# Kernel tuning notes

Hardware: AMD Instinct MI355X
Metric: run time of the kernel (lower is better)

Reference implementation:

```python
import jax, jax.numpy as jnp
import numpy as np

B, N, D_IN, D_OUT, H = 2, 2048, 1024, 1024, 16
HD = D_OUT // H


def setup_inputs() -> dict:
    key = jax.random.key(0)
    ks = jax.random.split(key, 6)
    s_in = 1.0 / np.sqrt(D_IN)
    s_out = 1.0 / np.sqrt(D_OUT)
    return {
        "x": jax.random.normal(ks[0], (B, N, D_IN), dtype=jnp.float32),
        "Wq": jax.random.uniform(ks[1], (D_IN, D_OUT), jnp.float32, -s_in, s_in),
        "Wk": jax.random.uniform(ks[2], (D_IN, D_OUT), jnp.float32, -s_in, s_in),
        "Wv": jax.random.uniform(ks[3], (D_IN, D_OUT), jnp.float32, -s_in, s_in),
        "Wo": jax.random.uniform(ks[4], (D_OUT, D_OUT), jnp.float32, -s_out, s_out),
        "bo": jax.random.uniform(ks[5], (D_OUT,), jnp.float32, -s_out, s_out),
    }


def reference(x, Wq, Wk, Wv, Wo, bo):
    b, n, _ = x.shape
    # project and split heads: [b, n, d_out] -> [b, h, n, hd]
    def heads(w):
        return w.reshape(b, n, H, HD).transpose(0, 2, 1, 3)
    q = heads(x @ Wq)
    k = heads(x @ Wk)
    v = heads(x @ Wv)
    # materialized causal attention (dropout rate 0.0 -> identity)
    scores = jnp.einsum("bhqd,bhkd->bhqk", q, k)
    causal = jnp.tril(jnp.ones((n, n), dtype=bool))  # keep lower triangle
    scores = jnp.where(causal, scores, -jnp.inf)
    attn = jax.nn.softmax(scores / np.sqrt(HD), axis=-1)
    ctx = jnp.einsum("bhqk,bhkd->bhqd", attn, v)
    ctx = ctx.transpose(0, 2, 1, 3).reshape(b, n, D_OUT)
    return ctx @ Wo + bo
```

## Files before the change

kernel.cpp:

```cpp
#include <hip/hip_runtime.h>
#include <math.h>
#include <stdint.h>

#define B_ 2
#define N_ 2048
#define D_ 1024
#define H_ 16
#define HD_ 64
#define M_ (B_ * N_)

typedef __bf16 bf16x8 __attribute__((ext_vector_type(8)));
typedef float f32x4 __attribute__((ext_vector_type(4)));

__device__ __forceinline__ ushort bfbits(float f) {
    __bf16 h = (__bf16)f;
    return __builtin_bit_cast(ushort, h);
}

__device__ __forceinline__ void glds16(const ushort* g, ushort* l) {
    __builtin_amdgcn_global_load_lds(
        (const __attribute__((address_space(1))) uint32_t*)g,
        (__attribute__((address_space(3))) uint32_t*)l, 16, 0, 0);
}

__global__ __launch_bounds__(256) void cvt_x(const float* __restrict__ x,
                                             ushort* __restrict__ xb) {
    int i = blockIdx.x * 256 + threadIdx.x;
    float4 v = ((const float4*)x)[i];
    ushort4 o;
    o.x = bfbits(v.x); o.y = bfbits(v.y); o.z = bfbits(v.z); o.w = bfbits(v.w);
    ((ushort4*)xb)[i] = o;
}

__global__ __launch_bounds__(256) void cvt_w(const float* __restrict__ W0,
                                             const float* __restrict__ W1,
                                             const float* __restrict__ W2,
                                             const float* __restrict__ W3,
                                             ushort* __restrict__ Wt) {
    __shared__ float T[32][33];
    const float* W = (blockIdx.z == 0) ? W0 : (blockIdx.z == 1) ? W1
                   : (blockIdx.z == 2) ? W2 : W3;
    ushort* out = Wt + (size_t)blockIdx.z * D_ * D_;
    const int t = threadIdx.x;
    const int k0 = blockIdx.x * 32, n0 = blockIdx.y * 32;
    {
        int kl = t >> 3, nl = (t & 7) * 4;
        float4 v = *(const float4*)&W[(size_t)(k0 + kl) * D_ + n0 + nl];
        T[kl][nl] = v.x; T[kl][nl + 1] = v.y; T[kl][nl + 2] = v.z; T[kl][nl + 3] = v.w;
    }
    __syncthreads();
    {
        int nl = t >> 3, k4 = (t & 7) * 4;
        ushort4 o;
        o.x = bfbits(T[k4 + 0][nl]); o.y = bfbits(T[k4 + 1][nl]);
        o.z = bfbits(T[k4 + 2][nl]); o.w = bfbits(T[k4 + 3][nl]);
        *(ushort4*)&out[(size_t)(n0 + nl) * D_ + k0 + k4] = o;
    }
}

#define BK 32

__device__ __forceinline__ void gemm_tile(const ushort* __restrict__ A,
                                          const ushort* __restrict__ Bt,
                                          int K, int tileM, int tileN,
                                          ushort* As, ushort* Bs,
                                          f32x4 acc[4][4]) {
    const int t = threadIdx.x;
    const int l = t & 63;
    const int w = __builtin_amdgcn_readfirstlane(t >> 6);
    const int wr = w >> 1, wc = w & 1;
    const int li = l & 15, lg = l >> 4;
    const int lr = l >> 2;
    const int colu = (((l & 3) ^ (lr & 3)) << 3);
    const int swz = (li & 3) << 3;

    for (int k0 = 0; k0 < K; k0 += BK) {
        __syncthreads();
        #pragma unroll
        for (int it = 0; it < 2; ++it) {
            const int c2 = it * 4 + w;
            const int row = c2 * 16 + lr;
            glds16(&A[(size_t)(tileM + row) * K + k0 + colu], &As[c2 * 512]);
            glds16(&Bt[(size_t)(tileN + row) * K + k0 + colu], &Bs[c2 * 512]);
        }
        __syncthreads();
        bf16x8 a[4], b[4];
        #pragma unroll
        for (int m = 0; m < 4; ++m)
            a[m] = *(const bf16x8*)&As[(wr * 64 + m * 16 + li) * 32 + ((lg << 3) ^ swz)];
        #pragma unroll
        for (int n = 0; n < 4; ++n)
            b[n] = *(const bf16x8*)&Bs[(wc * 64 + n * 16 + li) * 32 + ((lg << 3) ^ swz)];
        #pragma unroll
        for (int m = 0; m < 4; ++m)
            #pragma unroll
            for (int n = 0; n < 4; ++n)
                acc[m][n] = __builtin_amdgcn_mfma_f32_16x16x32_bf16(a[m], b[n], acc[m][n], 0, 0, 0);
    }
}

#define QSCALE 0.180336880f

__global__ __launch_bounds__(256) void qkv_gemm(const ushort* __restrict__ xb,
                                                const ushort* __restrict__ Wt,
                                                ushort* __restrict__ q,
                                                ushort* __restrict__ k,
                                                ushort* __restrict__ vt) {
    __shared__ ushort As[128 * 32];
    __shared__ ushort Bs[128 * 32];
    __shared__ ushort Eps[128][130];
    f32x4 acc[4][4];
    #pragma unroll
    for (int m = 0; m < 4; ++m)
        #pragma unroll
        for (int n = 0; n < 4; ++n)
            acc[m][n] = (f32x4){0.f, 0.f, 0.f, 0.f};

    const int tileM = blockIdx.x * 128;
    const int wsel = blockIdx.y >> 3;
    const int tileN = (blockIdx.y & 7) * 128;
    const ushort* Bmat = Wt + (size_t)wsel * D_ * D_;

    gemm_tile(xb, Bmat, D_, tileM, tileN, As, Bs, acc);

    const int t = threadIdx.x;
    const int l = t & 63, w = t >> 6;
    const int wr = w >> 1, wc = w & 1;
    const int li = l & 15, lg = l >> 4;
    const float scale = (wsel == 0) ? QSCALE : 1.0f;

    if (wsel < 2) {
        #pragma unroll
        for (int m = 0; m < 4; ++m)
            #pragma unroll
            for (int n = 0; n < 4; ++n)
                #pragma unroll
                for (int r = 0; r < 4; ++r)
                    Eps[wr * 64 + m * 16 + lg * 4 + r][wc * 64 + n * 16 + li] =
                        bfbits(acc[m][n][r] * scale);
    } else {
        #pragma unroll
        for (int m = 0; m < 4; ++m)
            #pragma unroll
            for (int n = 0; n < 4; ++n)
                #pragma unroll
                for (int r = 0; r < 4; ++r)
                    Eps[wc * 64 + n * 16 + li][wr * 64 + m * 16 + lg * 4 + r] =
                        bfbits(acc[m][n][r]);
    }
    __syncthreads();

    const int rr = t >> 3;
    const int cb = (t & 7) * 16;
    if (wsel < 2) {
        ushort* out = (wsel == 0) ? q : k;
        #pragma unroll
        for (int it = 0; it < 4; ++it) {
            const int row = it * 32 + rr;
            uint4 v0 = *(const uint4*)&Eps[row][cb];
            uint4 v1 = *(const uint4*)&Eps[row][cb + 8];
            size_t base = (size_t)(tileM + row) * D_ + tileN + cb;
            *(uint4*)&out[base] = v0;
            *(uint4*)&out[base + 8] = v1;
        }
    } else {
        const int b = tileM >> 11;
        const int n0 = (tileM & (N_ - 1)) + cb;
        #pragma unroll
        for (int it = 0; it < 4; ++it) {
            const int row = it * 32 + rr;
            const int gcol = tileN + row;
            const int h = gcol >> 6, hd = gcol & 63;
            uint4 v0 = *(const uint4*)&Eps[row][cb];
            uint4 v1 = *(const uint4*)&Eps[row][cb + 8];
            size_t base = ((size_t)(b * H_ + h) * HD_ + hd) * N_ + n0;
            *(uint4*)&vt[base] = v0;
            *(uint4*)&vt[base + 8] = v1;
        }
    }
}

__global__ __launch_bounds__(256) void out_gemm(const ushort* __restrict__ ctx,
                                                const ushort* __restrict__ Wt,
                                                const float* __restrict__ bo,
                                                float* __restrict__ outp) {
    __shared__ ushort As[128 * 32];
    __shared__ ushort Bs[128 * 32];
    __shared__ float Epf[32][132];
    f32x4 acc[4][4];
    #pragma unroll
    for (int m = 0; m < 4; ++m)
        #pragma unroll
        for (int n = 0; n < 4; ++n)
            acc[m][n] = (f32x4){0.f, 0.f, 0.f, 0.f};

    const int tileM = blockIdx.x * 128;
    const int tileN = blockIdx.y * 128;
    const ushort* Bmat = Wt + (size_t)3 * D_ * D_;

    gemm_tile(ctx, Bmat, D_, tileM, tileN, As, Bs, acc);

    const int t = threadIdx.x;
    const int l = t & 63, w = t >> 6;
    const int wr = w >> 1, wc = w & 1;
    const int li = l & 15, lg = l >> 4;
    const int lrow = t & 31;
    const int coff = (t >> 5) * 16;

    float bias[4];
    #pragma unroll
    for (int n = 0; n < 4; ++n) bias[n] = bo[tileN + wc * 64 + n * 16 + li];

    #pragma unroll
    for (int m = 0; m < 4; ++m) {
        __syncthreads();
        #pragma unroll
        for (int n = 0; n < 4; ++n)
            #pragma unroll
            for (int r = 0; r < 4; ++r)
                Epf[wr * 16 + lg * 4 + r][wc * 64 + n * 16 + li] = acc[m][n][r] + bias[n];
        __syncthreads();
        const int grow = tileM + (lrow >> 4) * 64 + m * 16 + (lrow & 15);
        #pragma unroll
        for (int j = 0; j < 4; ++j) {
            float4 vv = *(const float4*)&Epf[lrow][coff + j * 4];
            *(float4*)&outp[(size_t)grow * D_ + tileN + coff + j * 4] = vv;
        }
    }
}

__device__ __forceinline__ void qk_mfma(f32x4 st[4], const ushort* Kb,
                                        const bf16x8 bq[2],
                                        int li, int lg, int rswz) {
    #pragma unroll
    for (int c = 0; c < 4; ++c) {
        st[c] = (f32x4){0.f, 0.f, 0.f, 0.f};
        #pragma unroll
        for (int tk = 0; tk < 2; ++tk) {
            bf16x8 kf = *(const bf16x8*)&Kb[(c * 16 + li) * 64 + (((tk * 4 + lg) ^ rswz) * 8)];
            st[c] = __builtin_amdgcn_mfma_f32_16x16x32_bf16(kf, bq[tk], st[c], 0, 0, 0);
        }
    }
}

__device__ __forceinline__ void softmax_pv(f32x4 st[4], const ushort* Vb,
                                           bool masked, int jkb, int qg,
                                           int li, int lg, int rswz,
                                           ushort* PsW, f32x4& lacc,
                                           f32x4 od[4], bf16x8 ones) {
    if (masked) {
        #pragma unroll
        for (int c = 0; c < 4; ++c)
            #pragma unroll
            for (int r = 0; r < 4; ++r) {
                const int kgl = jkb * 64 + c * 16 + lg * 4 + r;
                if (kgl > qg) st[c][r] = -INFINITY;
            }
    }
    const int sw = li & 7;
    #pragma unroll
    for (int c = 0; c < 4; ++c) {
        float p0 = exp2f(st[c][0]);
        float p1 = exp2f(st[c][1]);
        float p2 = exp2f(st[c][2]);
        float p3 = exp2f(st[c][3]);
        uint32_t w0, w1;
        asm("v_cvt_pk_bf16_f32 %0, %1, %2" : "=v"(w0) : "v"(p0), "v"(p1));
        asm("v_cvt_pk_bf16_f32 %0, %1, %2" : "=v"(w1) : "v"(p2), "v"(p3));
        uint2 pk; pk.x = w0; pk.y = w1;
        *(uint2*)&PsW[li * 64 + (((c * 2 + (lg >> 1)) ^ sw) << 3) + ((lg & 1) << 2)] = pk;
    }
    #pragma unroll
    for (int tj = 0; tj < 2; ++tj) {
        bf16x8 pa = *(const bf16x8*)&PsW[li * 64 + (((tj * 4 + lg) ^ sw) << 3)];
        lacc = __builtin_amdgcn_mfma_f32_16x16x32_bf16(pa, ones, lacc, 0, 0, 0);
        #pragma unroll
        for (int db = 0; db < 4; ++db) {
            bf16x8 bv = *(const bf16x8*)&Vb[(db * 16 + li) * 64 + (((tj * 4 + lg) ^ rswz) * 8)];
            od[db] = __builtin_amdgcn_mfma_f32_16x16x32_bf16(pa, bv, od[db], 0, 0, 0);
        }
    }
}

__global__ __launch_bounds__(256, 4) void attn_fwd(const ushort* __restrict__ q,
                                                   const ushort* __restrict__ k,
                                                   const ushort* __restrict__ vt,
                                                   ushort* __restrict__ ctx) {
    __shared__ ushort Ks[2][4096];
    __shared__ ushort Vs[2][4096];
    __shared__ ushort Ps[4][1024];

    const int t = threadIdx.x;
    const int l = t & 63;
    const int w = __builtin_amdgcn_readfirstlane(t >> 6);
    const int li = l & 15, lg = l >> 4;
    const int f = blockIdx.x;
    const int bh = ((f & 7) << 2) | ((f >> 3) & 3);
    const int qt = 31 - (f >> 5);
    const int b = bh >> 4, h = bh & 15;

    const ushort* Qg = q + ((size_t)b * N_) * D_ + h * 64;
    const ushort* Kg = k + ((size_t)b * N_) * D_ + h * 64;
    const ushort* Vg = vt + (size_t)bh * HD_ * N_;
    ushort* PsW = &Ps[w][0];

    const int r8 = l >> 3;
    const int soff = ((l & 7) ^ r8) * 8;
    const int rswz = li & 7;

    const int qb64 = qt * 64 + w * 16;
    const int qg = qb64 + li;

    bf16x8 bq[2];
    #pragma unroll
    for (int tk = 0; tk < 2; ++tk)
        bq[tk] = *(const bf16x8*)&Qg[(size_t)qg * D_ + tk * 32 + lg * 8];

    bf16x8 ones;
    #pragma unroll
    for (int i = 0; i < 8; ++i) ones[i] = (__bf16)1.0f;

    f32x4 od[4];
    #pragma unroll
    for (int db = 0; db < 4; ++db) od[db] = (f32x4){0.f, 0.f, 0.f, 0.f};
    f32x4 lacc = (f32x4){0.f, 0.f, 0.f, 0.f};

    #pragma unroll
    for (int i = 0; i < 2; ++i) {
        const int seg = w + i * 4;
        const int row = seg * 8 + r8;
        glds16(&Kg[(size_t)row * D_ + soff], &Ks[0][seg * 512]);
        glds16(&Vg[(size_t)row * N_ + soff], &Vs[0][seg * 512]);
    }
    __syncthreads();

    int cur = 0;
    for (int kb = 0; kb < qt; ++kb) {
        #pragma unroll
        for (int i = 0; i < 2; ++i) {
            const int seg = w + i * 4;
            const int row = seg * 8 + r8;
            glds16(&Kg[(size_t)((kb + 1) * 64 + row) * D_ + soff], &Ks[cur ^ 1][seg * 512]);
            glds16(&Vg[(size_t)row * N_ + (kb + 1) * 64 + soff], &Vs[cur ^ 1][seg * 512]);
        }
        f32x4 st[4];
        qk_mfma(st, Ks[cur], bq, li, lg, rswz);
        softmax_pv(st, Vs[cur], false, kb, qg, li, lg, rswz, PsW, lacc, od, ones);
        __syncthreads();
        cur ^= 1;
    }
    {
        f32x4 st[4];
        qk_mfma(st, Ks[cur], bq, li, lg, rswz);
        softmax_pv(st, Vs[cur], true, qt, qg, li, lg, rswz, PsW, lacc, od, ones);
    }

    #pragma unroll
    for (int r = 0; r < 4; ++r) {
        const float inv = 1.f / lacc[r];
        const int grow = qb64 + lg * 4 + r;
        #pragma unroll
        for (int db = 0; db < 4; ++db)
            ctx[((size_t)(b * N_ + grow)) * D_ + h * 64 + db * 16 + li] = bfbits(od[db][r] * inv);
    }
}

extern "C" void kernel_launch(void* const* d_in, const int* in_sizes, int n_in,
                              void* d_out, int out_size, void* d_ws, size_t ws_size,
                              hipStream_t stream) {
    (void)in_sizes; (void)n_in; (void)out_size; (void)ws_size;
    const float* x  = (const float*)d_in[0];
    const float* Wq = (const float*)d_in[1];
    const float* Wk = (const float*)d_in[2];
    const float* Wv = (const float*)d_in[3];
    const float* Wo = (const float*)d_in[4];
    const float* bo = (const float*)d_in[5];
    float* outp = (float*)d_out;

    ushort* xb  = (ushort*)d_ws;
    ushort* Wt  = xb + (size_t)M_ * D_;
    ushort* qb  = Wt + (size_t)4 * D_ * D_;
    ushort* kb  = qb + (size_t)M_ * D_;
    ushort* vtb = kb + (size_t)M_ * D_;
    ushort* ctx = vtb + (size_t)M_ * D_;

    cvt_x<<<dim3((M_ * D_ / 4) / 256), 256, 0, stream>>>(x, xb);
    cvt_w<<<dim3(32, 32, 4), 256, 0, stream>>>(Wq, Wk, Wv, Wo, Wt);
    qkv_gemm<<<dim3(32, 24), 256, 0, stream>>>(xb, Wt, qb, kb, vtb);
    attn_fwd<<<dim3(1024), 256, 0, stream>>>(qb, kb, vtb, ctx);
    out_gemm<<<dim3(32, 8), 256, 0, stream>>>(ctx, Wt, bo, outp);
}
```

Measured before the change: 111.8 us.

## Pair causal query tiles per block, fuse conversion kernels, remap GEMM tiles

```diff
diff --git a/kernel.cpp b/kernel.cpp
--- a/kernel.cpp
+++ b/kernel.cpp
@@ -23,26 +23,29 @@
         (__attribute__((address_space(3))) uint32_t*)l, 16, 0, 0);
 }
 
-__global__ __launch_bounds__(256) void cvt_x(const float* __restrict__ x,
-                                             ushort* __restrict__ xb) {
-    int i = blockIdx.x * 256 + threadIdx.x;
-    float4 v = ((const float4*)x)[i];
-    ushort4 o;
-    o.x = bfbits(v.x); o.y = bfbits(v.y); o.z = bfbits(v.z); o.w = bfbits(v.w);
-    ((ushort4*)xb)[i] = o;
-}
-
-__global__ __launch_bounds__(256) void cvt_w(const float* __restrict__ W0,
-                                             const float* __restrict__ W1,
-                                             const float* __restrict__ W2,
-                                             const float* __restrict__ W3,
-                                             ushort* __restrict__ Wt) {
+__global__ __launch_bounds__(256) void prep(const float* __restrict__ x,
+                                            const float* __restrict__ W0,
+                                            const float* __restrict__ W1,
+                                            const float* __restrict__ W2,
+                                            const float* __restrict__ W3,
+                                            ushort* __restrict__ xb,
+                                            ushort* __restrict__ Wt) {
     __shared__ float T[32][33];
-    const float* W = (blockIdx.z == 0) ? W0 : (blockIdx.z == 1) ? W1
-                   : (blockIdx.z == 2) ? W2 : W3;
-    ushort* out = Wt + (size_t)blockIdx.z * D_ * D_;
     const int t = threadIdx.x;
-    const int k0 = blockIdx.x * 32, n0 = blockIdx.y * 32;
+    int id = blockIdx.x;
+    if (id < 4096) {
+        int i = id * 256 + t;
+        float4 v = ((const float4*)x)[i];
+        ushort4 o;
+        o.x = bfbits(v.x); o.y = bfbits(v.y); o.z = bfbits(v.z); o.w = bfbits(v.w);
+        ((ushort4*)xb)[i] = o;
+        return;
+    }
+    id -= 4096;
+    const int z = id >> 10;
+    const int k0 = (id & 31) * 32, n0 = ((id >> 5) & 31) * 32;
+    const float* W = (z == 0) ? W0 : (z == 1) ? W1 : (z == 2) ? W2 : W3;
+    ushort* out = Wt + (size_t)z * D_ * D_;
     {
         int kl = t >> 3, nl = (t & 7) * 4;
         float4 v = *(const float4*)&W[(size_t)(k0 + kl) * D_ + n0 + nl];
@@ -116,9 +119,11 @@
         for (int n = 0; n < 4; ++n)
             acc[m][n] = (f32x4){0.f, 0.f, 0.f, 0.f};
 
-    const int tileM = blockIdx.x * 128;
-    const int wsel = blockIdx.y >> 3;
-    const int tileN = (blockIdx.y & 7) * 128;
+    const int wg = (blockIdx.x & 7) * 96 + (blockIdx.x >> 3);
+    const int tileM = (wg & 31) * 128;
+    const int yy = wg >> 5;
+    const int wsel = yy >> 3;
+    const int tileN = (yy & 7) * 128;
     const ushort* Bmat = Wt + (size_t)wsel * D_ * D_;
 
     gemm_tile(xb, Bmat, D_, tileM, tileN, As, Bs, acc);
@@ -186,7 +191,6 @@
                                                 float* __restrict__ outp) {
     __shared__ ushort As[128 * 32];
     __shared__ ushort Bs[128 * 32];
-    __shared__ float Epf[32][132];
     f32x4 acc[4][4];
     #pragma unroll
     for (int m = 0; m < 4; ++m)
@@ -194,38 +198,27 @@
         for (int n = 0; n < 4; ++n)
             acc[m][n] = (f32x4){0.f, 0.f, 0.f, 0.f};
 
-    const int tileM = blockIdx.x * 128;
-    const int tileN = blockIdx.y * 128;
+    const int wg = (blockIdx.x & 7) * 32 + (blockIdx.x >> 3);
+    const int tileM = (wg & 31) * 128;
+    const int tileN = (wg >> 5) * 128;
     const ushort* Bmat = Wt + (size_t)3 * D_ * D_;
 
     gemm_tile(ctx, Bmat, D_, tileM, tileN, As, Bs, acc);
 
-    const int t = threadIdx.x;
-    const int l = t & 63, w = t >> 6;
+    const int l = threadIdx.x & 63, w = threadIdx.x >> 6;
     const int wr = w >> 1, wc = w & 1;
     const int li = l & 15, lg = l >> 4;
-    const int lrow = t & 31;
-    const int coff = (t >> 5) * 16;
-
-    float bias[4];
-    #pragma unroll
-    for (int n = 0; n < 4; ++n) bias[n] = bo[tileN + wc * 64 + n * 16 + li];
-
-    #pragma unroll
-    for (int m = 0; m < 4; ++m) {
-        __syncthreads();
-        #pragma unroll
-        for (int n = 0; n < 4; ++n)
-            #pragma unroll
-            for (int r = 0; r < 4; ++r)
-                Epf[wr * 16 + lg * 4 + r][wc * 64 + n * 16 + li] = acc[m][n][r] + bias[n];
-        __syncthreads();
-        const int grow = tileM + (lrow >> 4) * 64 + m * 16 + (lrow & 15);
-        #pragma unroll
-        for (int j = 0; j < 4; ++j) {
-            float4 vv = *(const float4*)&Epf[lrow][coff + j * 4];
-            *(float4*)&outp[(size_t)grow * D_ + tileN + coff + j * 4] = vv;
-        }
+    #pragma unroll
+    for (int n = 0; n < 4; ++n) {
+        float bias = bo[tileN + wc * 64 + n * 16 + li];
+        #pragma unroll
+        for (int m = 0; m < 4; ++m)
+            #pragma unroll
+            for (int r = 0; r < 4; ++r) {
+                int grow = tileM + wr * 64 + m * 16 + lg * 4 + r;
+                int gcol = tileN + wc * 64 + n * 16 + li;
+                outp[(size_t)grow * D_ + gcol] = acc[m][n][r] + bias;
+            }
     }
 }
 
@@ -282,7 +275,7 @@
     }
 }
 
-__global__ __launch_bounds__(256, 4) void attn_fwd(const ushort* __restrict__ q,
+__global__ __launch_bounds__(256, 2) void attn_fwd(const ushort* __restrict__ q,
                                                    const ushort* __restrict__ k,
                                                    const ushort* __restrict__ vt,
                                                    ushort* __restrict__ ctx) {
@@ -296,7 +289,8 @@
     const int li = l & 15, lg = l >> 4;
     const int f = blockIdx.x;
     const int bh = ((f & 7) << 2) | ((f >> 3) & 3);
-    const int qt = 31 - (f >> 5);
+    const int p = f >> 5;
+    const int qtA = p, qtB = 31 - p;
     const int b = bh >> 4, h = bh & 15;
 
     const ushort* Qg = q + ((size_t)b * N_) * D_ + h * 64;
@@ -308,22 +302,28 @@
     const int soff = ((l & 7) ^ r8) * 8;
     const int rswz = li & 7;
 
-    const int qb64 = qt * 64 + w * 16;
-    const int qg = qb64 + li;
-
-    bf16x8 bq[2];
-    #pragma unroll
-    for (int tk = 0; tk < 2; ++tk)
-        bq[tk] = *(const bf16x8*)&Qg[(size_t)qg * D_ + tk * 32 + lg * 8];
+    const int qgA = qtA * 64 + w * 16 + li;
+    const int qgB = qtB * 64 + w * 16 + li;
+
+    bf16x8 bqA[2], bqB[2];
+    #pragma unroll
+    for (int tk = 0; tk < 2; ++tk) {
+        bqA[tk] = *(const bf16x8*)&Qg[(size_t)qgA * D_ + tk * 32 + lg * 8];
+        bqB[tk] = *(const bf16x8*)&Qg[(size_t)qgB * D_ + tk * 32 + lg * 8];
+    }
 
     bf16x8 ones;
     #pragma unroll
     for (int i = 0; i < 8; ++i) ones[i] = (__bf16)1.0f;
 
-    f32x4 od[4];
-    #pragma unroll
-    for (int db = 0; db < 4; ++db) od[db] = (f32x4){0.f, 0.f, 0.f, 0.f};
-    f32x4 lacc = (f32x4){0.f, 0.f, 0.f, 0.f};
+    f32x4 odA[4], odB[4];
+    #pragma unroll
+    for (int db = 0; db < 4; ++db) {
+        odA[db] = (f32x4){0.f, 0.f, 0.f, 0.f};
+        odB[db] = (f32x4){0.f, 0.f, 0.f, 0.f};
+    }
+    f32x4 laccA = (f32x4){0.f, 0.f, 0.f, 0.f};
+    f32x4 laccB = (f32x4){0.f, 0.f, 0.f, 0.f};
 
     #pragma unroll
     for (int i = 0; i < 2; ++i) {
@@ -335,33 +335,42 @@
     __syncthreads();
 
     int cur = 0;
-    for (int kb = 0; kb < qt; ++kb) {
-        #pragma unroll
-        for (int i = 0; i < 2; ++i) {
-            const int seg = w + i * 4;
-            const int row = seg * 8 + r8;
-            glds16(&Kg[(size_t)((kb + 1) * 64 + row) * D_ + soff], &Ks[cur ^ 1][seg * 512]);
-            glds16(&Vg[(size_t)row * N_ + (kb + 1) * 64 + soff], &Vs[cur ^ 1][seg * 512]);
-        }
-        f32x4 st[4];
-        qk_mfma(st, Ks[cur], bq, li, lg, rswz);
-        softmax_pv(st, Vs[cur], false, kb, qg, li, lg, rswz, PsW, lacc, od, ones);
+    for (int kb = 0; kb <= qtB; ++kb) {
+        if (kb < qtB) {
+            #pragma unroll
+            for (int i = 0; i < 2; ++i) {
+                const int seg = w + i * 4;
+                const int row = seg * 8 + r8;
+                glds16(&Kg[(size_t)((kb + 1) * 64 + row) * D_ + soff], &Ks[cur ^ 1][seg * 512]);
+                glds16(&Vg[(size_t)row * N_ + (kb + 1) * 64 + soff], &Vs[cur ^ 1][seg * 512]);
+            }
+        }
+        {
+            f32x4 st[4];
+            qk_mfma(st, Ks[cur], bqB, li, lg, rswz);
+            softmax_pv(st, Vs[cur], kb == qtB, kb, qgB, li, lg, rswz, PsW, laccB, odB, ones);
+        }
+        if (kb <= qtA) {
+            f32x4 st[4];
+            qk_mfma(st, Ks[cur], bqA, li, lg, rswz);
+            softmax_pv(st, Vs[cur], kb == qtA, kb, qgA, li, lg, rswz, PsW, laccA, odA, ones);
+        }
         __syncthreads();
         cur ^= 1;
     }
-    {
-        f32x4 st[4];
-        qk_mfma(st, Ks[cur], bq, li, lg, rswz);
-        softmax_pv(st, Vs[cur], true, qt, qg, li, lg, rswz, PsW, lacc, od, ones);
-    }
 
     #pragma unroll
     for (int r = 0; r < 4; ++r) {
-        const float inv = 1.f / lacc[r];
-        const int grow = qb64 + lg * 4 + r;
+        const float invA = 1.f / laccA[r];
+        const int growA = qtA * 64 + w * 16 + lg * 4 + r;
         #pragma unroll
         for (int db = 0; db < 4; ++db)
-            ctx[((size_t)(b * N_ + grow)) * D_ + h * 64 + db * 16 + li] = bfbits(od[db][r] * inv);
+            ctx[((size_t)(b * N_ + growA)) * D_ + h * 64 + db * 16 + li] = bfbits(odA[db][r] * invA);
+        const float invB = 1.f / laccB[r];
+        const int growB = qtB * 64 + w * 16 + lg * 4 + r;
+        #pragma unroll
+        for (int db = 0; db < 4; ++db)
+            ctx[((size_t)(b * N_ + growB)) * D_ + h * 64 + db * 16 + li] = bfbits(odB[db][r] * invB);
     }
 }
 
@@ -384,9 +393,8 @@
     ushort* vtb = kb + (size_t)M_ * D_;
     ushort* ctx = vtb + (size_t)M_ * D_;
 
-    cvt_x<<<dim3((M_ * D_ / 4) / 256), 256, 0, stream>>>(x, xb);
-    cvt_w<<<dim3(32, 32, 4), 256, 0, stream>>>(Wq, Wk, Wv, Wo, Wt);
-    qkv_gemm<<<dim3(32, 24), 256, 0, stream>>>(xb, Wt, qb, kb, vtb);
-    attn_fwd<<<dim3(1024), 256, 0, stream>>>(qb, kb, vtb, ctx);
-    out_gemm<<<dim3(32, 8), 256, 0, stream>>>(ctx, Wt, bo, outp);
-}
+    prep<<<dim3(8192), 256, 0, stream>>>(x, Wq, Wk, Wv, Wo, xb, Wt);
+    qkv_gemm<<<dim3(768), 256, 0, stream>>>(xb, Wt, qb, kb, vtb);
+    attn_fwd<<<dim3(512), 256, 0, stream>>>(qb, kb, vtb, ctx);
+    out_gemm<<<dim3(256), 256, 0, stream>>>(ctx, Wt, bo, outp);
+}
```

Measured after the change: 106.8 us. 1.05x faster.
